# Optimization experiments

Hardware: AMD Instinct MI355X
Metric: run time of the kernel (lower is better)

The kernel has to match this reference:

```python
import jax, jax.numpy as jnp
import numpy as np

B, L, R, D = 4, 1024, 4, 1024   # batch, seq, expansion rate, model dim
HEADS, HD, FF = 16, 64, 4096
EPS = 1e-6


def _static_alpha(layer_id):
    a0 = np.zeros((R, 1), np.float32)
    a0[layer_id % R, 0] = 1.0
    return jnp.asarray(np.concatenate([a0, np.eye(R, dtype=np.float32)], axis=1))  # [R, R+1]


def setup_inputs() -> dict:
    key = jax.random.key(0)
    ks = jax.random.split(key, 12)
    w = lambda k, shape, s=0.02: (jax.random.normal(k, shape, jnp.float32) * s)
    return {
        "H": jax.random.normal(ks[0], (B, L, R, D), jnp.float32),
        # attention hyper-connection (layer_id*2 = 0)
        "hc1_norm_w": jnp.ones((D,), jnp.float32),
        "hc1_alpha_fn": w(ks[1], (D, R + 1), 0.01),
        "hc1_beta_fn": w(ks[2], (D,), 0.01),
        "hc1_a_scale": jnp.full((1,), 0.01, jnp.float32),
        "hc1_b_scale": jnp.full((1,), 0.01, jnp.float32),
        "hc1_s_alpha": _static_alpha(0),
        "hc1_s_beta": jnp.ones((R,), jnp.float32),
        # attention
        "attn_norm_w": jnp.ones((D,), jnp.float32),
        "qkv_w": w(ks[3], (3 * D, D)),
        "out_w": w(ks[4], (D, D)),
        # ffn hyper-connection (layer_id*2+1 = 1)
        "hc2_norm_w": jnp.ones((D,), jnp.float32),
        "hc2_alpha_fn": w(ks[5], (D, R + 1), 0.01),
        "hc2_beta_fn": w(ks[6], (D,), 0.01),
        "hc2_a_scale": jnp.full((1,), 0.01, jnp.float32),
        "hc2_b_scale": jnp.full((1,), 0.01, jnp.float32),
        "hc2_s_alpha": _static_alpha(1),
        "hc2_s_beta": jnp.ones((R,), jnp.float32),
        # ffn
        "ffn_norm_w": jnp.ones((D,), jnp.float32),
        "fc1_w": w(ks[7], (FF, D)),
        "fc2_w": w(ks[8], (D, FF)),
    }


def _rms(x, weight):
    norm = jnp.sqrt(jnp.mean(x * x, axis=-1, keepdims=True))
    return weight * x / (norm + EPS)


def _width(Hm, norm_w, alpha_fn, beta_fn, a_scale, b_scale, s_alpha, s_beta):
    nh = _rms(Hm, norm_w)                                      # [B,L,R,D]
    alpha = jnp.tanh(jnp.einsum('blnd,dk->blnk', nh, alpha_fn)) * a_scale + s_alpha  # [B,L,R,R+1]
    beta = jnp.tanh(jnp.einsum('blnd,d->bln', nh, beta_fn)) * b_scale + s_beta       # [B,L,R]
    mix = jnp.einsum('blnk,blnd->blkd', alpha, Hm)             # [B,L,R+1,D]
    return mix, beta


def _depth(mix, out, beta):
    return beta[..., None] * out[:, :, None, :] + mix[..., 1:, :]


def _attention(x, qkv_w, out_w):
    b, l, d = x.shape
    qkv = (x @ qkv_w.T).reshape(b, l, 3, HEADS, HD)
    q, k, v = (jnp.moveaxis(qkv, 2, 0)[i].transpose(0, 2, 1, 3) for i in range(3))  # [B,H,L,HD]
    scores = jnp.einsum('bhqd,bhkd->bhqk', q, k) * (HD ** -0.5)
    causal = jnp.tril(jnp.ones((l, l), bool))
    scores = jnp.where(causal, scores, jnp.float32(-jnp.inf))
    attn = jax.nn.softmax(scores, axis=-1)
    out = jnp.einsum('bhqk,bhkd->bhqd', attn, v).transpose(0, 2, 1, 3).reshape(b, l, d)
    return out @ out_w.T


def reference(H, hc1_norm_w, hc1_alpha_fn, hc1_beta_fn, hc1_a_scale, hc1_b_scale,
              hc1_s_alpha, hc1_s_beta, attn_norm_w, qkv_w, out_w,
              hc2_norm_w, hc2_alpha_fn, hc2_beta_fn, hc2_a_scale, hc2_b_scale,
              hc2_s_alpha, hc2_s_beta, ffn_norm_w, fc1_w, fc2_w):
    # attention block
    mix, beta = _width(H, hc1_norm_w, hc1_alpha_fn, hc1_beta_fn,
                       hc1_a_scale, hc1_b_scale, hc1_s_alpha, hc1_s_beta)
    h = _rms(mix[..., 0, :], attn_norm_w)
    h = _attention(h, qkv_w, out_w)
    H = _depth(mix, h, beta)
    # ffn block
    mix, beta = _width(H, hc2_norm_w, hc2_alpha_fn, hc2_beta_fn,
                       hc2_a_scale, hc2_b_scale, hc2_s_alpha, hc2_s_beta)
    h = _rms(mix[..., 0, :], ffn_norm_w)
    h = (jax.nn.gelu(h @ fc1_w.T, approximate=False)) @ fc2_w.T
    H = _depth(mix, h, beta)
    return H
```

## Files before the change

### kernel.cpp

```cpp
#include <hip/hip_runtime.h>
#include <math.h>

#define BB 4
#define LL 1024
#define RR 4
#define DD 1024
#define NHEADS 16
#define HDIM 64
#define FFD 4096
#define EPSV 1e-6f

typedef short s16x8 __attribute__((ext_vector_type(8)));
typedef float f32x4 __attribute__((ext_vector_type(4)));
typedef unsigned short u16;

__device__ inline unsigned short f2bf(float x) {
  unsigned u = __builtin_bit_cast(unsigned, x);
  unsigned r = (u + 0x7fffu + ((u >> 16) & 1u)) >> 16;
  return (unsigned short)r;
}
__device__ inline float bf2f(u16 x) {
  return __builtin_bit_cast(float, (unsigned)x << 16);
}

__device__ inline float wred_sum(float v) {
#pragma unroll
  for (int off = 32; off; off >>= 1) v += __shfl_down(v, off);
  return v;
}

__device__ inline void gload_lds16(const u16* g, u16* l) {
  __builtin_amdgcn_global_load_lds(
      (const __attribute__((address_space(1))) unsigned int*)g,
      (__attribute__((address_space(3))) unsigned int*)l, 16, 0, 0);
}

__global__ __launch_bounds__(256) void cvt4_kernel(
    const float* __restrict__ s0, const float* __restrict__ s1,
    const float* __restrict__ s2, const float* __restrict__ s3,
    u16* __restrict__ d0, u16* __restrict__ d1,
    u16* __restrict__ d2, u16* __restrict__ d3) {
  const int n0 = 786432, n1 = 262144, n2 = 1048576, n3 = 1048576;
  const int total = n0 + n1 + n2 + n3;
  for (int i = blockIdx.x * 256 + threadIdx.x; i < total; i += gridDim.x * 256) {
    const float4* src; ushort4* dst; int j;
    if (i < n0)                { src = (const float4*)s0; dst = (ushort4*)d0; j = i; }
    else if (i < n0 + n1)      { src = (const float4*)s1; dst = (ushort4*)d1; j = i - n0; }
    else if (i < n0 + n1 + n2) { src = (const float4*)s2; dst = (ushort4*)d2; j = i - n0 - n1; }
    else                       { src = (const float4*)s3; dst = (ushort4*)d3; j = i - n0 - n1 - n2; }
    float4 v = src[j];
    ushort4 o;
    o.x = f2bf(v.x); o.y = f2bf(v.y); o.z = f2bf(v.z); o.w = f2bf(v.w);
    dst[j] = o;
  }
}

template<int NP>
__global__ __launch_bounds__(256) void width_kernel(
    const float* __restrict__ Hin,
    const u16* mixrest_in,
    const float* __restrict__ beta_in,
    const u16* __restrict__ pp,
    const float* __restrict__ hc_norm_w,
    const float* __restrict__ alpha_fn,
    const float* __restrict__ beta_fn,
    const float* __restrict__ a_scale,
    const float* __restrict__ b_scale,
    const float* __restrict__ s_alpha,
    const float* __restrict__ s_beta,
    const float* __restrict__ post_norm_w,
    u16* mixrest_out,
    float* __restrict__ beta_out,
    u16* __restrict__ x_out)
{
  const size_t MN = (size_t)4096 * 1024;
  const int bl = blockIdx.x;
  const int t = threadIdx.x;
  const int wid = t >> 6;
  __shared__ __align__(16) float Hs[4 * 1024];
  __shared__ __align__(16) float m0[1024];
  __shared__ float scr[96];
  __shared__ float alpha_s[4][5];
  __shared__ float beta_s[4];
  __shared__ float inv_s[4];
  __shared__ float inv0_s;

  if (NP > 0) {
    int d0 = t * 4;
    float4 s; s.x = 0.f; s.y = 0.f; s.z = 0.f; s.w = 0.f;
#pragma unroll
    for (int p = 0; p < (NP > 0 ? NP : 1); ++p) {
      ushort4 v = *(const ushort4*)&pp[p * MN + (size_t)bl * 1024 + d0];
      s.x += bf2f(v.x); s.y += bf2f(v.y); s.z += bf2f(v.z); s.w += bf2f(v.w);
    }
    ((float4*)m0)[t] = s;
    __syncthreads();
    for (int i = t; i < 1024; i += 256) {
      int n = i >> 8;
      float be = beta_in[bl * 4 + n];
      ushort4 mr = ((const ushort4*)(mixrest_in + (size_t)bl * 4096))[i];
      float4 ao = ((const float4*)m0)[i & 255];
      float4 hv;
      hv.x = be * ao.x + bf2f(mr.x); hv.y = be * ao.y + bf2f(mr.y);
      hv.z = be * ao.z + bf2f(mr.z); hv.w = be * ao.w + bf2f(mr.w);
      ((float4*)Hs)[i] = hv;
    }
  } else {
    for (int i = t; i < 1024; i += 256)
      ((float4*)Hs)[i] = ((const float4*)(Hin + (size_t)bl * 4096))[i];
  }
  __syncthreads();

  float ss[4];
#pragma unroll
  for (int n = 0; n < 4; ++n) {
    float a = 0.f;
    for (int d = t; d < 1024; d += 256) { float v = Hs[n * 1024 + d]; a += v * v; }
    ss[n] = a;
  }
#pragma unroll
  for (int n = 0; n < 4; ++n) {
    float r = wred_sum(ss[n]);
    if ((t & 63) == 0) scr[wid * 4 + n] = r;
  }
  __syncthreads();
  if (t < 4) {
    float tot = scr[t] + scr[4 + t] + scr[8 + t] + scr[12 + t];
    inv_s[t] = 1.f / (sqrtf(tot * (1.f / 1024.f)) + EPSV);
  }
  __syncthreads();
  float inv[4] = {inv_s[0], inv_s[1], inv_s[2], inv_s[3]};

  float dots[4][6];
#pragma unroll
  for (int n = 0; n < 4; ++n)
#pragma unroll
    for (int k = 0; k < 6; ++k) dots[n][k] = 0.f;
  for (int d = t; d < 1024; d += 256) {
    float w = hc_norm_w[d];
    float a0 = alpha_fn[d * 5 + 0], a1 = alpha_fn[d * 5 + 1], a2 = alpha_fn[d * 5 + 2],
          a3 = alpha_fn[d * 5 + 3], a4 = alpha_fn[d * 5 + 4];
    float bfv = beta_fn[d];
#pragma unroll
    for (int n = 0; n < 4; ++n) {
      float nh = Hs[n * 1024 + d] * w * inv[n];
      dots[n][0] += nh * a0; dots[n][1] += nh * a1; dots[n][2] += nh * a2;
      dots[n][3] += nh * a3; dots[n][4] += nh * a4; dots[n][5] += nh * bfv;
    }
  }
  __syncthreads();
#pragma unroll
  for (int n = 0; n < 4; ++n)
#pragma unroll
    for (int k = 0; k < 6; ++k) {
      float r = wred_sum(dots[n][k]);
      if ((t & 63) == 0) scr[wid * 24 + n * 6 + k] = r;
    }
  __syncthreads();
  if (t < 24) {
    float raw = scr[t] + scr[24 + t] + scr[48 + t] + scr[72 + t];
    int n = t / 6, k = t % 6;
    if (k < 5) alpha_s[n][k] = tanhf(raw) * a_scale[0] + s_alpha[n * 5 + k];
    else       beta_s[n]     = tanhf(raw) * b_scale[0] + s_beta[n];
  }
  __syncthreads();

  {
    int i = t;
    float4 h0 = ((const float4*)Hs)[i];
    float4 h1 = ((const float4*)Hs)[256 + i];
    float4 h2 = ((const float4*)Hs)[512 + i];
    float4 h3 = ((const float4*)Hs)[768 + i];
#pragma unroll
    for (int k = 0; k < 5; ++k) {
      float c0 = alpha_s[0][k], c1 = alpha_s[1][k], c2 = alpha_s[2][k], c3 = alpha_s[3][k];
      float4 mv;
      mv.x = c0 * h0.x + c1 * h1.x + c2 * h2.x + c3 * h3.x;
      mv.y = c0 * h0.y + c1 * h1.y + c2 * h2.y + c3 * h3.y;
      mv.z = c0 * h0.z + c1 * h1.z + c2 * h2.z + c3 * h3.z;
      mv.w = c0 * h0.w + c1 * h1.w + c2 * h2.w + c3 * h3.w;
      if (k == 0) {
        ((float4*)m0)[i] = mv;
      } else {
        ushort4 ov;
        ov.x = f2bf(mv.x); ov.y = f2bf(mv.y); ov.z = f2bf(mv.z); ov.w = f2bf(mv.w);
        ((ushort4*)(mixrest_out + (size_t)bl * 4096 + (size_t)(k - 1) * 1024))[i] = ov;
      }
    }
  }
  if (t < 4) beta_out[bl * 4 + t] = beta_s[t];
  __syncthreads();

  {
    float a = 0.f;
    for (int d = t; d < 1024; d += 256) { float v = m0[d]; a += v * v; }
    float r = wred_sum(a);
    if ((t & 63) == 0) scr[wid] = r;
  }
  __syncthreads();
  if (t == 0) {
    float tot = scr[0] + scr[1] + scr[2] + scr[3];
    inv0_s = 1.f / (sqrtf(tot * (1.f / 1024.f)) + EPSV);
  }
  __syncthreads();
  {
    float iv = inv0_s;
    float4 mv = ((const float4*)m0)[t];
    float4 wv = ((const float4*)post_norm_w)[t];
    ushort4 ov;
    ov.x = f2bf(wv.x * mv.x * iv);
    ov.y = f2bf(wv.y * mv.y * iv);
    ov.z = f2bf(wv.z * mv.z * iv);
    ov.w = f2bf(wv.w * mv.w * iv);
    ((ushort4*)(x_out + (size_t)bl * 1024))[t] = ov;
  }
}

template<int EPI, int SPLIT>
__global__ __launch_bounds__(256, 4) void gemm_bt_kernel(
    const u16* __restrict__ A, const u16* __restrict__ W,
    u16* __restrict__ Cb, u16* __restrict__ Vt,
    int M, int N, int K)
{
  __shared__ __align__(16) u16 LDSb[2][2][128 * 32];
  const int tn = N >> 7, tm = M >> 7;
  int bid = blockIdx.x;
  const int nwg = gridDim.x;
  if ((nwg & 7) == 0) bid = (bid & 7) * (nwg >> 3) + (bid >> 3);
  const int ts = tm * tn;
  const int sK = bid / ts;
  const int tb = bid - sK * ts;
  const int bm = tb / tn, bn = tb % tn;
  const int Kc = K / SPLIT;
  const int kbeg = sK * Kc;

  const int t = threadIdx.x, l = t & 63, w = t >> 6;
  const int wr = w >> 1, wc = w & 1;
  const int m0 = bm << 7, n0 = bn << 7;
  const int ssc = (((l & 3) ^ ((l >> 3) & 3)) << 3);
  const int srA = m0 + (w << 5) + (l >> 2);
  const int srB = n0 + (w << 5) + (l >> 2);
  const int ldso = (w << 10);
  const int fr = l & 15, g4 = l >> 4;
  const int fc8 = ((g4 ^ ((l >> 1) & 3)) << 3);

  f32x4 acc[4][4];
#pragma unroll
  for (int i = 0; i < 4; ++i)
#pragma unroll
    for (int j = 0; j < 4; ++j)
#pragma unroll
      for (int e = 0; e < 4; ++e) acc[i][j][e] = 0.f;

  const u16* pa0 = A + (size_t)srA * K + kbeg + ssc;
  const u16* pa1 = A + (size_t)(srA + 16) * K + kbeg + ssc;
  const u16* pb0 = W + (size_t)srB * K + kbeg + ssc;
  const u16* pb1 = W + (size_t)(srB + 16) * K + kbeg + ssc;

#define STAGE(buf, koff)                                   \
  do {                                                     \
    gload_lds16(pa0 + (koff), &LDSb[buf][0][ldso]);        \
    gload_lds16(pa1 + (koff), &LDSb[buf][0][ldso + 512]);  \
    gload_lds16(pb0 + (koff), &LDSb[buf][1][ldso]);        \
    gload_lds16(pb1 + (koff), &LDSb[buf][1][ldso + 512]);  \
  } while (0)

  const int nt = Kc >> 5;
  STAGE(0, 0);
  int cur = 0;
  for (int kt = 0; kt < nt; ++kt) {
    if (kt + 1 < nt) {
      STAGE(cur ^ 1, (kt + 1) << 5);
      asm volatile("s_waitcnt vmcnt(4)" ::: "memory");
    } else {
      asm volatile("s_waitcnt vmcnt(0)" ::: "memory");
    }
    __builtin_amdgcn_s_barrier();
    __builtin_amdgcn_sched_barrier(0);
    s16x8 af[4], bfr[4];
#pragma unroll
    for (int m = 0; m < 4; ++m)
      af[m] = *(const s16x8*)(&LDSb[cur][0][(wr * 64 + m * 16 + fr) * 32 + fc8]);
#pragma unroll
    for (int n = 0; n < 4; ++n)
      bfr[n] = *(const s16x8*)(&LDSb[cur][1][(wc * 64 + n * 16 + fr) * 32 + fc8]);
#pragma unroll
    for (int m = 0; m < 4; ++m)
#pragma unroll
      for (int n = 0; n < 4; ++n)
        acc[m][n] = __builtin_amdgcn_mfma_f32_16x16x32_bf16(af[m], bfr[n], acc[m][n], 0, 0, 0);
    asm volatile("s_waitcnt lgkmcnt(0)" ::: "memory");
    __builtin_amdgcn_sched_barrier(0);
    __builtin_amdgcn_s_barrier();
    cur ^= 1;
  }
#undef STAGE

  if (EPI == 2 && n0 >= 2048) {
    const int rbv = m0 + wr * 64 + (g4 << 2);
    const int cbv = n0 + wc * 64 + fr;
#pragma unroll
    for (int m = 0; m < 4; ++m)
#pragma unroll
      for (int n = 0; n < 4; ++n) {
        int cc = cbv + n * 16 - 2048;
        int hh = cc >> 6, dd = cc & 63;
        int r0 = rbv + m * 16;
        ushort4 ov;
        ov.x = f2bf(acc[m][n][0]); ov.y = f2bf(acc[m][n][1]);
        ov.z = f2bf(acc[m][n][2]); ov.w = f2bf(acc[m][n][3]);
        *(ushort4*)&Vt[((size_t)((r0 >> 10) * 16 + hh) * 64 + dd) * 1024 + (r0 & 1023)] = ov;
      }
    return;
  }

  float* scr = (float*)LDSb;
  const int strideN = (EPI == 2) ? 2048 : N;
  u16* Cout = (SPLIT > 1) ? (Cb + (size_t)sK * M * N) : Cb;
#pragma unroll
  for (int r = 0; r < 2; ++r) {
    __syncthreads();
    if (wr == r) {
#pragma unroll
      for (int m = 0; m < 4; ++m)
#pragma unroll
        for (int n = 0; n < 4; ++n)
#pragma unroll
          for (int j = 0; j < 4; ++j) {
            int lr = m * 16 + (g4 << 2) + j;
            int col = wc * 64 + n * 16 + fr;
            scr[lr * 128 + (col ^ ((((lr >> 2) & 7)) << 3))] = acc[m][n][j];
          }
    }
    __syncthreads();
#pragma unroll
    for (int it = 0; it < 4; ++it) {
      int lr = it * 16 + (t >> 4);
      int key8 = ((lr >> 2) & 7) << 3;
      int lc = (t & 15) << 3;
      int cb0 = (lc ^ key8);
      f32x4 v0 = *(const f32x4*)&scr[lr * 128 + cb0];
      f32x4 v1 = *(const f32x4*)&scr[lr * 128 + cb0 + 4];
      float vv[8] = {v0[0], v0[1], v0[2], v0[3], v1[0], v1[1], v1[2], v1[3]};
      s16x8 ov;
#pragma unroll
      for (int c = 0; c < 8; ++c) {
        float v = vv[c];
        if (EPI == 1) v = 0.5f * v * (1.f + erff(v * 0.70710678118f));
        ov[c] = (short)f2bf(v);
      }
      size_t gr = (size_t)(m0 + r * 64 + lr);
      *(s16x8*)&Cout[gr * strideN + n0 + lc] = ov;
    }
  }
}

__global__ __launch_bounds__(256) void attn_mfma_kernel(
    const u16* __restrict__ qk, const u16* __restrict__ Vt, u16* __restrict__ out)
{
  const int id = blockIdx.x;
  const int hb = id & 63, qt0 = id >> 6;
  const int b = hb >> 4, h = hb & 15;
  const int qt = (h & 1) ? (15 - qt0) : qt0;
  const int t = threadIdx.x, l = t & 63, w = t >> 6;
  const int q0 = qt << 6;
  __shared__ __align__(16) u16 Ks[2][64 * 64];
  __shared__ __align__(16) u16 Vs[2][64 * 64];
  __shared__ __align__(16) u16 Ps[4][16 * 64];

  const int fr = l & 15;
  const int fg = (l >> 4) << 3;
  const int fswz = (fr & 7) << 3;

  const int qrow = q0 + w * 16 + fr;
  const size_t qbase = (size_t)(b * 1024 + qrow) * 2048 + h * 64 + fg;
  const s16x8 aq0 = *(const s16x8*)(qk + qbase);
  const s16x8 aq1 = *(const s16x8*)(qk + qbase + 32);

  f32x4 acc_o[4];
#pragma unroll
  for (int i = 0; i < 4; ++i)
#pragma unroll
    for (int e = 0; e < 4; ++e) acc_o[i][e] = 0.f;
  float m_i[4] = {-INFINITY, -INFINITY, -INFINITY, -INFINITY};
  float l_i[4] = {0.f, 0.f, 0.f, 0.f};

  const int sr = (w << 3) + (l >> 3);
  const int scs = (((l & 7) ^ ((l >> 3) & 7)) << 3);
  const u16* ksrc = qk + (size_t)(b * 1024 + sr) * 2048 + 1024 + h * 64 + scs;
  const u16* vsrc = Vt + ((size_t)((b * 16 + h) * 64 + sr)) * 1024 + scs;
  const int ldst = (w << 9);

#define ASTAGE(buf, kb_)                                                     \
  do {                                                                       \
    gload_lds16(ksrc + (size_t)(kb_) * 2048, &Ks[buf][ldst]);                \
    gload_lds16(ksrc + (size_t)((kb_) + 32) * 2048, &Ks[buf][2048 + ldst]);  \
    gload_lds16(vsrc + (kb_), &Vs[buf][ldst]);                               \
    gload_lds16(vsrc + (kb_) + 32 * 1024, &Vs[buf][2048 + ldst]);            \
  } while (0)

  const int qrow_c = q0 + w * 16 + ((l >> 4) << 2);
  u16* Psw = &Ps[w][0];
  const int nkt = qt + 1;

  ASTAGE(0, 0);
  int cur = 0;
  for (int kt = 0; kt < nkt; ++kt) {
    const int kb = kt << 6;
    if (kt + 1 < nkt) {
      ASTAGE(cur ^ 1, (kt + 1) << 6);
      asm volatile("s_waitcnt vmcnt(4)" ::: "memory");
    } else {
      asm volatile("s_waitcnt vmcnt(0)" ::: "memory");
    }
    __builtin_amdgcn_s_barrier();
    __builtin_amdgcn_sched_barrier(0);

    f32x4 s[4];
#pragma unroll
    for (int n = 0; n < 4; ++n) {
#pragma unroll
      for (int e = 0; e < 4; ++e) s[n][e] = 0.f;
      s16x8 bk0 = *(const s16x8*)(&Ks[cur][(n * 16 + fr) * 64 + (fg ^ fswz)]);
      s16x8 bk1 = *(const s16x8*)(&Ks[cur][(n * 16 + fr) * 64 + ((32 + fg) ^ fswz)]);
      s[n] = __builtin_amdgcn_mfma_f32_16x16x32_bf16(aq0, bk0, s[n], 0, 0, 0);
      s[n] = __builtin_amdgcn_mfma_f32_16x16x32_bf16(aq1, bk1, s[n], 0, 0, 0);
    }
#pragma unroll
    for (int n = 0; n < 4; ++n)
#pragma unroll
      for (int e = 0; e < 4; ++e) s[n][e] *= 0.125f;
    if (kt == nkt - 1 && kb == q0) {
#pragma unroll
      for (int n = 0; n < 4; ++n) {
        int kc = kb + n * 16 + fr;
#pragma unroll
        for (int r = 0; r < 4; ++r)
          if (kc > qrow_c + r) s[n][r] = -INFINITY;
      }
    }

    float rm[4], fac[4];
#pragma unroll
    for (int r = 0; r < 4; ++r)
      rm[r] = fmaxf(fmaxf(s[0][r], s[1][r]), fmaxf(s[2][r], s[3][r]));
#pragma unroll
    for (int off = 1; off < 16; off <<= 1)
#pragma unroll
      for (int r = 0; r < 4; ++r) rm[r] = fmaxf(rm[r], __shfl_xor(rm[r], off));
#pragma unroll
    for (int r = 0; r < 4; ++r) {
      float mn = fmaxf(m_i[r], rm[r]);
      fac[r] = __expf(m_i[r] - mn);
      m_i[r] = mn;
    }
    float rs[4] = {0.f, 0.f, 0.f, 0.f};
    float pb[4][4];
#pragma unroll
    for (int n = 0; n < 4; ++n)
#pragma unroll
      for (int r = 0; r < 4; ++r) {
        float pv = __expf(s[n][r] - m_i[r]);
        pb[n][r] = pv;
        rs[r] += pv;
      }
#pragma unroll
    for (int off = 1; off < 16; off <<= 1)
#pragma unroll
      for (int r = 0; r < 4; ++r) rs[r] += __shfl_xor(rs[r], off);
#pragma unroll
    for (int r = 0; r < 4; ++r) l_i[r] = l_i[r] * fac[r] + rs[r];
#pragma unroll
    for (int dt = 0; dt < 4; ++dt)
#pragma unroll
      for (int r = 0; r < 4; ++r) acc_o[dt][r] *= fac[r];

#pragma unroll
    for (int n = 0; n < 4; ++n)
#pragma unroll
      for (int r = 0; r < 4; ++r) {
        int prow = ((l >> 4) << 2) + r;
        Psw[prow * 64 + ((n * 16 + fr) ^ ((prow & 7) << 3))] = f2bf(pb[n][r]);
      }
    asm volatile("s_waitcnt lgkmcnt(0)" ::: "memory");
    __builtin_amdgcn_sched_barrier(0);

    s16x8 pa0 = *(const s16x8*)(Psw + fr * 64 + (fg ^ fswz));
    s16x8 pa1 = *(const s16x8*)(Psw + fr * 64 + ((32 + fg) ^ fswz));
#pragma unroll
    for (int dt = 0; dt < 4; ++dt) {
      s16x8 bv0 = *(const s16x8*)(&Vs[cur][(dt * 16 + fr) * 64 + (fg ^ fswz)]);
      s16x8 bv1 = *(const s16x8*)(&Vs[cur][(dt * 16 + fr) * 64 + ((32 + fg) ^ fswz)]);
      acc_o[dt] = __builtin_amdgcn_mfma_f32_16x16x32_bf16(pa0, bv0, acc_o[dt], 0, 0, 0);
      acc_o[dt] = __builtin_amdgcn_mfma_f32_16x16x32_bf16(pa1, bv1, acc_o[dt], 0, 0, 0);
    }
    asm volatile("s_waitcnt lgkmcnt(0)" ::: "memory");
    __builtin_amdgcn_sched_barrier(0);
    __builtin_amdgcn_s_barrier();
    cur ^= 1;
  }
#undef ASTAGE

  float invl[4];
#pragma unroll
  for (int r = 0; r < 4; ++r) invl[r] = 1.f / l_i[r];
#pragma unroll
  for (int dt = 0; dt < 4; ++dt)
#pragma unroll
    for (int r = 0; r < 4; ++r) {
      size_t idx = (size_t)(b * 1024 + qrow_c + r) * 1024 + h * 64 + dt * 16 + fr;
      out[idx] = f2bf(acc_o[dt][r] * invl[r]);
    }
}

template<int NPART>
__global__ __launch_bounds__(256) void depth2_kernel(
    const u16* __restrict__ parts, const u16* __restrict__ mixrest,
    const float* __restrict__ beta, float* __restrict__ Hout)
{
  const size_t MN = (size_t)4096 * 1024;
  const size_t stride = (size_t)gridDim.x * 256;
  const size_t n8 = (size_t)BB * LL * RR * DD / 8;
  for (size_t i = (size_t)blockIdx.x * 256 + threadIdx.x; i < n8; i += stride) {
    size_t e = i * 8;
    int d = (int)(e & 1023);
    int n = (int)((e >> 10) & 3);
    size_t bl = e >> 12;
    float be = beta[bl * 4 + n];
    float f[8];
#pragma unroll
    for (int j = 0; j < 8; ++j) f[j] = 0.f;
#pragma unroll
    for (int p = 0; p < NPART; ++p) {
      s16x8 v = *(const s16x8*)&parts[p * MN + bl * 1024 + d];
#pragma unroll
      for (int j = 0; j < 8; ++j) f[j] += bf2f((u16)v[j]);
    }
    s16x8 m = *(const s16x8*)&mixrest[e];
    float4 o0, o1;
    o0.x = be * f[0] + bf2f((u16)m[0]); o0.y = be * f[1] + bf2f((u16)m[1]);
    o0.z = be * f[2] + bf2f((u16)m[2]); o0.w = be * f[3] + bf2f((u16)m[3]);
    o1.x = be * f[4] + bf2f((u16)m[4]); o1.y = be * f[5] + bf2f((u16)m[5]);
    o1.z = be * f[6] + bf2f((u16)m[6]); o1.w = be * f[7] + bf2f((u16)m[7]);
    *(float4*)&Hout[e] = o0;
    *(float4*)&Hout[e + 4] = o1;
  }
}

extern "C" void kernel_launch(void* const* d_in, const int* in_sizes, int n_in,
                              void* d_out, int out_size, void* d_ws, size_t ws_size,
                              hipStream_t stream) {
  const float* H       = (const float*)d_in[0];
  const float* hc1_nw  = (const float*)d_in[1];
  const float* hc1_afn = (const float*)d_in[2];
  const float* hc1_bfn = (const float*)d_in[3];
  const float* hc1_as  = (const float*)d_in[4];
  const float* hc1_bs  = (const float*)d_in[5];
  const float* hc1_sa  = (const float*)d_in[6];
  const float* hc1_sb  = (const float*)d_in[7];
  const float* attn_nw = (const float*)d_in[8];
  const float* qkv_w   = (const float*)d_in[9];
  const float* out_w   = (const float*)d_in[10];
  const float* hc2_nw  = (const float*)d_in[11];
  const float* hc2_afn = (const float*)d_in[12];
  const float* hc2_bfn = (const float*)d_in[13];
  const float* hc2_as  = (const float*)d_in[14];
  const float* hc2_bs  = (const float*)d_in[15];
  const float* hc2_sa  = (const float*)d_in[16];
  const float* hc2_sb  = (const float*)d_in[17];
  const float* ffn_nw  = (const float*)d_in[18];
  const float* fc1_w   = (const float*)d_in[19];
  const float* fc2_w   = (const float*)d_in[20];
  float* Hout = (float*)d_out;

  char* wsp = (char*)d_ws;
  size_t off = 0;
  auto carve = [&](size_t bytes) {
    void* p = wsp + off;
    off = (off + bytes + 255) & ~(size_t)255;
    return p;
  };
  const size_t MN = (size_t)4096 * 1024;
  u16* wq_bf   = (u16*)carve((size_t)3072 * 1024 * 2);
  u16* wo_bf   = (u16*)carve((size_t)1024 * 1024 * 2);
  u16* w1_bf   = (u16*)carve((size_t)4096 * 1024 * 2);
  u16* w2_bf   = (u16*)carve((size_t)4096 * 1024 * 2);
  u16* xbf     = (u16*)carve((size_t)4096 * 1024 * 2);
  u16* mixrest = (u16*)carve((size_t)4096 * 4096 * 2);
  float* beta1 = (float*)carve((size_t)16384 * 4);
  float* beta2 = (float*)carve((size_t)16384 * 4);
  char* uregion = (char*)carve((size_t)32 * 1024 * 1024);
  u16* qk_bf   = (u16*)uregion;
  u16* Vt      = (u16*)(uregion + (size_t)16 * 1024 * 1024);
  u16* g1_bf   = (u16*)uregion;
  u16* attn_bf = (u16*)carve((size_t)4096 * 1024 * 2);
  u16* pp      = (u16*)carve((size_t)4 * MN * 2);

  cvt4_kernel<<<2048, 256, 0, stream>>>(qkv_w, out_w, fc1_w, fc2_w, wq_bf, wo_bf, w1_bf, w2_bf);
  width_kernel<0><<<4096, 256, 0, stream>>>(H, nullptr, nullptr, nullptr,
      hc1_nw, hc1_afn, hc1_bfn, hc1_as, hc1_bs, hc1_sa, hc1_sb, attn_nw,
      mixrest, beta1, xbf);
  gemm_bt_kernel<2, 1><<<768, 256, 0, stream>>>(xbf, wq_bf, qk_bf, Vt, 4096, 3072, 1024);
  attn_mfma_kernel<<<1024, 256, 0, stream>>>(qk_bf, Vt, attn_bf);
  gemm_bt_kernel<0, 4><<<1024, 256, 0, stream>>>(attn_bf, wo_bf, pp, nullptr, 4096, 1024, 1024);
  width_kernel<4><<<4096, 256, 0, stream>>>(nullptr, mixrest, beta1, pp,
      hc2_nw, hc2_afn, hc2_bfn, hc2_as, hc2_bs, hc2_sa, hc2_sb, ffn_nw,
      mixrest, beta2, xbf);
  gemm_bt_kernel<1, 1><<<1024, 256, 0, stream>>>(xbf, w1_bf, g1_bf, nullptr, 4096, 4096, 1024);
  gemm_bt_kernel<0, 4><<<1024, 256, 0, stream>>>(g1_bf, w2_bf, pp, nullptr, 4096, 1024, 4096);
  depth2_kernel<4><<<4096, 256, 0, stream>>>(pp, mixrest, beta2, Hout);
}
```

Baseline: 327.0 us.

## Restructure width kernel to one token per wavefront with register-resident data

The hyper-connection width kernel now gives each 64-lane wavefront one token, so a 256-thread block handles four tokens and the grid shrinks to a quarter. All H values stay in registers and every reduction is a wavefront xor-shuffle, which removes the shared-memory staging and the many block-wide barriers. The RMS scale is applied after the dot product, and the alpha_fn loads are vectorised. In exchange, register pressure per thread rises (64 floats of H plus 24 accumulators), which may lower occupancy.

After: 301.2 us. -7.9%, faster.

```diff
diff --git a/kernel.cpp b/kernel.cpp
--- a/kernel.cpp
+++ b/kernel.cpp
@@ -23,9 +23,9 @@
   return __builtin_bit_cast(float, (unsigned)x << 16);
 }
 
-__device__ inline float wred_sum(float v) {
-#pragma unroll
-  for (int off = 32; off; off >>= 1) v += __shfl_down(v, off);
+__device__ inline float wred_xor(float v) {
+#pragma unroll
+  for (int off = 1; off < 64; off <<= 1) v += __shfl_xor(v, off);
   return v;
 }
 
@@ -58,7 +58,7 @@
 template<int NP>
 __global__ __launch_bounds__(256) void width_kernel(
     const float* __restrict__ Hin,
-    const u16* mixrest_in,
+    const u16* __restrict__ mixrest_in,
     const float* __restrict__ beta_in,
     const u16* __restrict__ pp,
     const float* __restrict__ hc_norm_w,
@@ -69,150 +69,153 @@
     const float* __restrict__ s_alpha,
     const float* __restrict__ s_beta,
     const float* __restrict__ post_norm_w,
-    u16* mixrest_out,
+    u16* __restrict__ mixrest_out,
     float* __restrict__ beta_out,
     u16* __restrict__ x_out)
 {
   const size_t MN = (size_t)4096 * 1024;
-  const int bl = blockIdx.x;
-  const int t = threadIdx.x;
-  const int wid = t >> 6;
-  __shared__ __align__(16) float Hs[4 * 1024];
-  __shared__ __align__(16) float m0[1024];
-  __shared__ float scr[96];
-  __shared__ float alpha_s[4][5];
-  __shared__ float beta_s[4];
-  __shared__ float inv_s[4];
-  __shared__ float inv0_s;
-
+  const int l = threadIdx.x & 63, w = threadIdx.x >> 6;
+  const int bl = blockIdx.x * 4 + w;
+  const int d0 = l << 2;
+
+  float4 h[4][4];
   if (NP > 0) {
-    int d0 = t * 4;
-    float4 s; s.x = 0.f; s.y = 0.f; s.z = 0.f; s.w = 0.f;
-#pragma unroll
-    for (int p = 0; p < (NP > 0 ? NP : 1); ++p) {
-      ushort4 v = *(const ushort4*)&pp[p * MN + (size_t)bl * 1024 + d0];
-      s.x += bf2f(v.x); s.y += bf2f(v.y); s.z += bf2f(v.z); s.w += bf2f(v.w);
-    }
-    ((float4*)m0)[t] = s;
-    __syncthreads();
-    for (int i = t; i < 1024; i += 256) {
-      int n = i >> 8;
-      float be = beta_in[bl * 4 + n];
-      ushort4 mr = ((const ushort4*)(mixrest_in + (size_t)bl * 4096))[i];
-      float4 ao = ((const float4*)m0)[i & 255];
-      float4 hv;
-      hv.x = be * ao.x + bf2f(mr.x); hv.y = be * ao.y + bf2f(mr.y);
-      hv.z = be * ao.z + bf2f(mr.z); hv.w = be * ao.w + bf2f(mr.w);
-      ((float4*)Hs)[i] = hv;
+    float be[4];
+#pragma unroll
+    for (int n = 0; n < 4; ++n) be[n] = beta_in[bl * 4 + n];
+#pragma unroll
+    for (int i = 0; i < 4; ++i) {
+      const int d = i * 256 + d0;
+      float4 s; s.x = 0.f; s.y = 0.f; s.z = 0.f; s.w = 0.f;
+#pragma unroll
+      for (int p = 0; p < (NP > 0 ? NP : 1); ++p) {
+        ushort4 v = *(const ushort4*)&pp[p * MN + (size_t)bl * 1024 + d];
+        s.x += bf2f(v.x); s.y += bf2f(v.y); s.z += bf2f(v.z); s.w += bf2f(v.w);
+      }
+#pragma unroll
+      for (int n = 0; n < 4; ++n) {
+        ushort4 mr = *(const ushort4*)&mixrest_in[(size_t)bl * 4096 + n * 1024 + d];
+        h[n][i].x = be[n] * s.x + bf2f(mr.x);
+        h[n][i].y = be[n] * s.y + bf2f(mr.y);
+        h[n][i].z = be[n] * s.z + bf2f(mr.z);
+        h[n][i].w = be[n] * s.w + bf2f(mr.w);
+      }
     }
   } else {
-    for (int i = t; i < 1024; i += 256)
-      ((float4*)Hs)[i] = ((const float4*)(Hin + (size_t)bl * 4096))[i];
-  }
-  __syncthreads();
-
-  float ss[4];
+#pragma unroll
+    for (int i = 0; i < 4; ++i) {
+      const int d = i * 256 + d0;
+#pragma unroll
+      for (int n = 0; n < 4; ++n)
+        h[n][i] = *(const float4*)&Hin[(size_t)bl * 4096 + n * 1024 + d];
+    }
+  }
+
+  float inv[4];
 #pragma unroll
   for (int n = 0; n < 4; ++n) {
     float a = 0.f;
-    for (int d = t; d < 1024; d += 256) { float v = Hs[n * 1024 + d]; a += v * v; }
-    ss[n] = a;
-  }
+#pragma unroll
+    for (int i = 0; i < 4; ++i)
+      a += h[n][i].x * h[n][i].x + h[n][i].y * h[n][i].y +
+           h[n][i].z * h[n][i].z + h[n][i].w * h[n][i].w;
+    a = wred_xor(a);
+    inv[n] = 1.f / (sqrtf(a * (1.f / 1024.f)) + EPSV);
+  }
+
+  float dots[4][6];
+#pragma unroll
+  for (int n = 0; n < 4; ++n)
+#pragma unroll
+    for (int k = 0; k < 6; ++k) dots[n][k] = 0.f;
+#pragma unroll
+  for (int i = 0; i < 4; ++i) {
+    const int d = i * 256 + d0;
+    float4 nw = *(const float4*)&hc_norm_w[d];
+    float4 bfv4 = *(const float4*)&beta_fn[d];
+    float4 A0 = *(const float4*)&alpha_fn[d * 5];
+    float4 A1 = *(const float4*)&alpha_fn[d * 5 + 4];
+    float4 A2 = *(const float4*)&alpha_fn[d * 5 + 8];
+    float4 A3 = *(const float4*)&alpha_fn[d * 5 + 12];
+    float4 A4 = *(const float4*)&alpha_fn[d * 5 + 16];
+    const float af[4][5] = {
+        {A0.x, A0.y, A0.z, A0.w, A1.x},
+        {A1.y, A1.z, A1.w, A2.x, A2.y},
+        {A2.z, A2.w, A3.x, A3.y, A3.z},
+        {A3.w, A4.x, A4.y, A4.z, A4.w}};
+    const float nwv[4] = {nw.x, nw.y, nw.z, nw.w};
+    const float bfl[4] = {bfv4.x, bfv4.y, bfv4.z, bfv4.w};
+#pragma unroll
+    for (int j = 0; j < 4; ++j) {
+      const float wj = nwv[j];
+#pragma unroll
+      for (int n = 0; n < 4; ++n) {
+        const float hw = (j == 0 ? h[n][i].x : j == 1 ? h[n][i].y : j == 2 ? h[n][i].z : h[n][i].w) * wj;
+        dots[n][0] += hw * af[j][0];
+        dots[n][1] += hw * af[j][1];
+        dots[n][2] += hw * af[j][2];
+        dots[n][3] += hw * af[j][3];
+        dots[n][4] += hw * af[j][4];
+        dots[n][5] += hw * bfl[j];
+      }
+    }
+  }
+  const float as = a_scale[0], bs = b_scale[0];
+  float alpha[4][5], betav[4];
 #pragma unroll
   for (int n = 0; n < 4; ++n) {
-    float r = wred_sum(ss[n]);
-    if ((t & 63) == 0) scr[wid * 4 + n] = r;
-  }
-  __syncthreads();
-  if (t < 4) {
-    float tot = scr[t] + scr[4 + t] + scr[8 + t] + scr[12 + t];
-    inv_s[t] = 1.f / (sqrtf(tot * (1.f / 1024.f)) + EPSV);
-  }
-  __syncthreads();
-  float inv[4] = {inv_s[0], inv_s[1], inv_s[2], inv_s[3]};
-
-  float dots[4][6];
-#pragma unroll
-  for (int n = 0; n < 4; ++n)
-#pragma unroll
-    for (int k = 0; k < 6; ++k) dots[n][k] = 0.f;
-  for (int d = t; d < 1024; d += 256) {
-    float w = hc_norm_w[d];
-    float a0 = alpha_fn[d * 5 + 0], a1 = alpha_fn[d * 5 + 1], a2 = alpha_fn[d * 5 + 2],
-          a3 = alpha_fn[d * 5 + 3], a4 = alpha_fn[d * 5 + 4];
-    float bfv = beta_fn[d];
-#pragma unroll
-    for (int n = 0; n < 4; ++n) {
-      float nh = Hs[n * 1024 + d] * w * inv[n];
-      dots[n][0] += nh * a0; dots[n][1] += nh * a1; dots[n][2] += nh * a2;
-      dots[n][3] += nh * a3; dots[n][4] += nh * a4; dots[n][5] += nh * bfv;
-    }
-  }
-  __syncthreads();
-#pragma unroll
-  for (int n = 0; n < 4; ++n)
-#pragma unroll
-    for (int k = 0; k < 6; ++k) {
-      float r = wred_sum(dots[n][k]);
-      if ((t & 63) == 0) scr[wid * 24 + n * 6 + k] = r;
-    }
-  __syncthreads();
-  if (t < 24) {
-    float raw = scr[t] + scr[24 + t] + scr[48 + t] + scr[72 + t];
-    int n = t / 6, k = t % 6;
-    if (k < 5) alpha_s[n][k] = tanhf(raw) * a_scale[0] + s_alpha[n * 5 + k];
-    else       beta_s[n]     = tanhf(raw) * b_scale[0] + s_beta[n];
-  }
-  __syncthreads();
-
-  {
-    int i = t;
-    float4 h0 = ((const float4*)Hs)[i];
-    float4 h1 = ((const float4*)Hs)[256 + i];
-    float4 h2 = ((const float4*)Hs)[512 + i];
-    float4 h3 = ((const float4*)Hs)[768 + i];
 #pragma unroll
     for (int k = 0; k < 5; ++k) {
-      float c0 = alpha_s[0][k], c1 = alpha_s[1][k], c2 = alpha_s[2][k], c3 = alpha_s[3][k];
+      float r = wred_xor(dots[n][k]);
+      alpha[n][k] = tanhf(r * inv[n]) * as + s_alpha[n * 5 + k];
+    }
+    float rb = wred_xor(dots[n][5]);
+    betav[n] = tanhf(rb * inv[n]) * bs + s_beta[n];
+  }
+  if (l == 0) {
+#pragma unroll
+    for (int n = 0; n < 4; ++n) beta_out[bl * 4 + n] = betav[n];
+  }
+
+  float4 mix0[4];
+#pragma unroll
+  for (int i = 0; i < 4; ++i) {
+    const int d = i * 256 + d0;
+#pragma unroll
+    for (int k = 0; k < 5; ++k) {
+      const float c0 = alpha[0][k], c1 = alpha[1][k], c2 = alpha[2][k], c3 = alpha[3][k];
       float4 mv;
-      mv.x = c0 * h0.x + c1 * h1.x + c2 * h2.x + c3 * h3.x;
-      mv.y = c0 * h0.y + c1 * h1.y + c2 * h2.y + c3 * h3.y;
-      mv.z = c0 * h0.z + c1 * h1.z + c2 * h2.z + c3 * h3.z;
-      mv.w = c0 * h0.w + c1 * h1.w + c2 * h2.w + c3 * h3.w;
+      mv.x = c0 * h[0][i].x + c1 * h[1][i].x + c2 * h[2][i].x + c3 * h[3][i].x;
+      mv.y = c0 * h[0][i].y + c1 * h[1][i].y + c2 * h[2][i].y + c3 * h[3][i].y;
+      mv.z = c0 * h[0][i].z + c1 * h[1][i].z + c2 * h[2][i].z + c3 * h[3][i].z;
+      mv.w = c0 * h[0][i].w + c1 * h[1][i].w + c2 * h[2][i].w + c3 * h[3][i].w;
       if (k == 0) {
-        ((float4*)m0)[i] = mv;
+        mix0[i] = mv;
       } else {
         ushort4 ov;
         ov.x = f2bf(mv.x); ov.y = f2bf(mv.y); ov.z = f2bf(mv.z); ov.w = f2bf(mv.w);
-        ((ushort4*)(mixrest_out + (size_t)bl * 4096 + (size_t)(k - 1) * 1024))[i] = ov;
-      }
-    }
-  }
-  if (t < 4) beta_out[bl * 4 + t] = beta_s[t];
-  __syncthreads();
-
-  {
-    float a = 0.f;
-    for (int d = t; d < 1024; d += 256) { float v = m0[d]; a += v * v; }
-    float r = wred_sum(a);
-    if ((t & 63) == 0) scr[wid] = r;
-  }
-  __syncthreads();
-  if (t == 0) {
-    float tot = scr[0] + scr[1] + scr[2] + scr[3];
-    inv0_s = 1.f / (sqrtf(tot * (1.f / 1024.f)) + EPSV);
-  }
-  __syncthreads();
-  {
-    float iv = inv0_s;
-    float4 mv = ((const float4*)m0)[t];
-    float4 wv = ((const float4*)post_norm_w)[t];
+        *(ushort4*)&mixrest_out[(size_t)bl * 4096 + (size_t)(k - 1) * 1024 + d] = ov;
+      }
+    }
+  }
+
+  float a0s = 0.f;
+#pragma unroll
+  for (int i = 0; i < 4; ++i)
+    a0s += mix0[i].x * mix0[i].x + mix0[i].y * mix0[i].y +
+           mix0[i].z * mix0[i].z + mix0[i].w * mix0[i].w;
+  a0s = wred_xor(a0s);
+  const float iv0 = 1.f / (sqrtf(a0s * (1.f / 1024.f)) + EPSV);
+#pragma unroll
+  for (int i = 0; i < 4; ++i) {
+    const int d = i * 256 + d0;
+    float4 pw = *(const float4*)&post_norm_w[d];
     ushort4 ov;
-    ov.x = f2bf(wv.x * mv.x * iv);
-    ov.y = f2bf(wv.y * mv.y * iv);
-    ov.z = f2bf(wv.z * mv.z * iv);
-    ov.w = f2bf(wv.w * mv.w * iv);
-    ((ushort4*)(x_out + (size_t)bl * 1024))[t] = ov;
+    ov.x = f2bf(pw.x * mix0[i].x * iv0);
+    ov.y = f2bf(pw.y * mix0[i].y * iv0);
+    ov.z = f2bf(pw.z * mix0[i].z * iv0);
+    ov.w = f2bf(pw.w * mix0[i].w * iv0);
+    *(ushort4*)&x_out[(size_t)bl * 1024 + d] = ov;
   }
 }
 
@@ -597,13 +600,13 @@
   u16* pp      = (u16*)carve((size_t)4 * MN * 2);
 
   cvt4_kernel<<<2048, 256, 0, stream>>>(qkv_w, out_w, fc1_w, fc2_w, wq_bf, wo_bf, w1_bf, w2_bf);
-  width_kernel<0><<<4096, 256, 0, stream>>>(H, nullptr, nullptr, nullptr,
+  width_kernel<0><<<1024, 256, 0, stream>>>(H, nullptr, nullptr, nullptr,
       hc1_nw, hc1_afn, hc1_bfn, hc1_as, hc1_bs, hc1_sa, hc1_sb, attn_nw,
       mixrest, beta1, xbf);
   gemm_bt_kernel<2, 1><<<768, 256, 0, stream>>>(xbf, wq_bf, qk_bf, Vt, 4096, 3072, 1024);
   attn_mfma_kernel<<<1024, 256, 0, stream>>>(qk_bf, Vt, attn_bf);
   gemm_bt_kernel<0, 4><<<1024, 256, 0, stream>>>(attn_bf, wo_bf, pp, nullptr, 4096, 1024, 1024);
-  width_kernel<4><<<4096, 256, 0, stream>>>(nullptr, mixrest, beta1, pp,
+  width_kernel<4><<<1024, 256, 0, stream>>>(nullptr, mixrest, beta1, pp,
       hc2_nw, hc2_afn, hc2_bfn, hc2_as, hc2_bs, hc2_sa, hc2_sb, ffn_nw,
       mixrest, beta2, xbf);
   gemm_bt_kernel<1, 1><<<1024, 256, 0, stream>>>(xbf, w1_bf, g1_bf, nullptr, 4096, 4096, 1024);
```
